# Kernel optimization log

Measured on AMD Instinct MI355X. Metric: run time of the kernel, lower is better.

Reference implementation:

```python
import jax, jax.numpy as jnp
import numpy as np

# Dimensions
N, C, D, H = 4, 1024, 768, 12      # docs, seq_len, hidden, heads
E, M, P = 32, 4, 256               # entities/doc, mentions/entity, pairs/doc
BS, NL = 64, 97                    # block_size, num relation labels


def setup_inputs() -> dict:
    key = jax.random.key(0)
    ks = jax.random.split(key, 16)
    s = 0.02
    seq = jax.random.normal(ks[0], (N, C, D), jnp.float32)
    attn = jax.random.uniform(ks[1], (N, H, C, C), jnp.float32)
    pos = jax.random.randint(ks[2], (N, E, M), 1, C)         # mention positions (offset applied, all valid)
    hts = jax.random.randint(ks[3], (N, P, 2), 0, E)         # entity-pair indices
    return {
        'seq': seq, 'attn': attn, 'pos': pos, 'hts': hts,
        'Wq': jax.random.normal(ks[4], (D, D), jnp.float32) * s,
        'bq': jnp.zeros((D,), jnp.float32),
        'Wk': jax.random.normal(ks[5], (D, D), jnp.float32) * s,
        'bk': jnp.zeros((D,), jnp.float32),
        'aw': jax.random.normal(ks[6], (2 * D, 1), jnp.float32) * s,
        'ab': jnp.zeros((1,), jnp.float32),
        'Wh': jax.random.normal(ks[7], (3 * D, D), jnp.float32) * s,
        'bh': jnp.zeros((D,), jnp.float32),
        'Wt': jax.random.normal(ks[8], (3 * D, D), jnp.float32) * s,
        'bt': jnp.zeros((D,), jnp.float32),
        'Wb': jax.random.normal(ks[9], (D * BS, NL), jnp.float32) * s,
        'bb': jnp.zeros((NL,), jnp.float32),
    }


def mention_guide(rs, mem, mask, Wq, bq, Wk, bk, aw, ab):
    # rs: [N,P,D] query; mem: [N,P,M,D] mention embs; mask: [N,P,M] bool
    sq = rs @ Wq + bq                                  # [N,P,D]
    sk = mem @ Wk + bk                                 # [N,P,M,D]
    sq_exp = jnp.broadcast_to(sq[:, :, None, :], sk.shape)
    inp = jnp.concatenate([sq_exp, sk], axis=-1)       # [N,P,M,2D]
    scores = jax.nn.leaky_relu((inp @ aw + ab)[..., 0], 0.01)   # [N,P,M]
    scores = jnp.where(mask, scores, -1e9)
    p = jax.nn.softmax(scores, axis=-1)                # attention over mentions
    return jnp.einsum('npm,npmd->npd', p, sk)


def reference(seq, attn, pos, hts, Wq, bq, Wk, bk, aw, ab, Wh, bh, Wt, bt, Wb, bb):
    nidx = jnp.arange(N)
    # per-entity mention gather + logsumexp pooling
    ment_emb = seq[nidx[:, None, None], pos]                      # [N,E,M,D]
    ent_emb = jax.scipy.special.logsumexp(ment_emb, axis=2)       # [N,E,D]
    att_t = attn.transpose(0, 2, 1, 3)                            # [N,C,H,C]
    ent_att = att_t[nidx[:, None, None], pos].mean(axis=2)        # [N,E,H,C]

    h_idx, t_idx = hts[..., 0], hts[..., 1]
    b = nidx[:, None]
    hs = ent_emb[b, h_idx]                                        # [N,P,D]
    ts = ent_emb[b, t_idx]
    h_att = ent_att[b, h_idx]                                     # [N,P,H,C]
    t_att = ent_att[b, t_idx]
    ht_att = (h_att * t_att).mean(axis=2)                         # [N,P,C]
    ht_att = ht_att / (ht_att.sum(axis=-1, keepdims=True) + 1e-5)
    rs = jnp.einsum('ncd,npc->npd', seq, ht_att)                  # local context

    # mention-level attention for head/tail entities
    h_pos = pos[b, h_idx]                                         # [N,P,M]
    t_pos = pos[b, t_idx]
    h_embs = seq[nidx[:, None, None], h_pos]                      # [N,P,M,D]
    t_embs = seq[nidx[:, None, None], t_pos]
    hess = mention_guide(rs, h_embs, h_pos != 0, Wq, bq, Wk, bk, aw, ab)
    tess = mention_guide(rs, t_embs, t_pos != 0, Wq, bq, Wk, bk, aw, ab)

    zh = jnp.tanh(jnp.tanh(jnp.concatenate([rs, hs, hess], -1) @ Wh + bh))
    zt = jnp.tanh(jnp.concatenate([rs, ts, tess], -1) @ Wt + bt)

    # group bilinear classifier
    b1 = zh.reshape(N * P, D // BS, BS)
    b2 = zt.reshape(N * P, D // BS, BS)
    bl = (b1[:, :, :, None] * b2[:, :, None, :]).reshape(N * P, D * BS)
    return bl @ Wb + bb                                            # [N*P, NL]
```

## Files before the change

### kernel.cpp

```cpp
#include <hip/hip_runtime.h>
#include <hip/hip_bf16.h>
#include <math.h>

#define N_ 4
#define C_ 1024
#define D_ 768
#define H_ 12
#define E_ 32
#define M_ 4
#define P_ 256
#define NL_ 97
#define NLP_ 112
#define NP_ (N_*P_)
#define K3D_ 2304
#define KBL_ 49152

typedef __attribute__((ext_vector_type(8))) short short8;
typedef __attribute__((ext_vector_type(4))) float f32x4;
typedef __attribute__((ext_vector_type(4))) unsigned short ushort4v;

__device__ __forceinline__ short f2bf(float x){
  union { __hip_bfloat16 h; short s; } u; u.h = __float2bfloat16(x); return u.s;
}
__device__ __forceinline__ unsigned short f2bfu(float x){
  union { __hip_bfloat16 h; unsigned short s; } u; u.h = __float2bfloat16(x); return u.s;
}
__device__ __forceinline__ float bf2f(unsigned short u){
  union { unsigned int i; float f; } x; x.i = ((unsigned int)u)<<16; return x.f;
}

__device__ __forceinline__ float blockReduceSum256(float v){
  __shared__ float red_s[4];
  #pragma unroll
  for (int o=32;o>0;o>>=1) v += __shfl_down(v, o);
  if ((threadIdx.x & 63)==0) red_s[threadIdx.x>>6] = v;
  __syncthreads();
  float t = red_s[0]+red_s[1]+red_s[2]+red_s[3];
  __syncthreads();
  return t;
}

__device__ __forceinline__ void tcvt64(const float* __restrict__ in,
    __hip_bfloat16* __restrict__ out, int R, int C, int Cp, int tile){
  __shared__ float tb[64][33];
  const int tiles_c = (Cp + 31) >> 5;
  const int rb = (tile/tiles_c)*64, cb = (tile%tiles_c)*32;
  const int tid = threadIdx.x;
  const bool vec = ((C & 3) == 0);
  #pragma unroll
  for (int i=0;i<2;i++){
    const int idx = tid + i*256;
    const int row = idx>>3, c4 = (idx&7)*4;
    const int c = cb + c4;
    float v0=0.f,v1=0.f,v2=0.f,v3=0.f;
    if (vec && c+3 < C){
      const f32x4 v = *(const f32x4*)&in[(size_t)(rb+row)*C + c];
      v0=v[0]; v1=v[1]; v2=v[2]; v3=v[3];
    } else {
      const float* rp = in + (size_t)(rb+row)*C;
      if (c   < C) v0 = rp[c];
      if (c+1 < C) v1 = rp[c+1];
      if (c+2 < C) v2 = rp[c+2];
      if (c+3 < C) v3 = rp[c+3];
    }
    tb[row][c4]=v0; tb[row][c4+1]=v1; tb[row][c4+2]=v2; tb[row][c4+3]=v3;
  }
  __syncthreads();
  #pragma unroll
  for (int i=0;i<4;i++){
    const int idx = tid + i*256;
    const int cr = idx>>5, p = idx&31;
    const int cc = cb + cr;
    if (cc < Cp){
      union { struct { unsigned short a,b; } s; unsigned int u; } pk;
      pk.s.a = f2bfu(tb[2*p][cr]);
      pk.s.b = f2bfu(tb[2*p+1][cr]);
      *(unsigned int*)&out[(size_t)cc*R + rb + 2*p] = pk.u;
    }
  }
}

#define T_WH 864
#define T_WT 864
#define T_WK 288
#define T_WB 3072
#define T_SEQ 1536
#define O_WT  (T_WH)
#define O_WK  (O_WT+T_WT)
#define O_WB  (O_WK+T_WK)
#define O_SEQ (O_WB+T_WB)
#define O_EMB (O_SEQ+T_SEQ)
#define O_ATT (O_EMB+N_*E_)
#define O_VQ  (O_ATT+N_*E_*H_)
#define O_WKAW (O_VQ+D_)
#define O_MISC (O_WKAW+D_)
#define G_PREP (O_MISC+1)

__global__ __launch_bounds__(256) void k_prep(
    const float* __restrict__ seq, const float* __restrict__ attn,
    const int* __restrict__ pos,
    const float* __restrict__ Wq, const float* __restrict__ bq,
    const float* __restrict__ Wk, const float* __restrict__ bk,
    const float* __restrict__ aw, const float* __restrict__ ab,
    const float* __restrict__ Wh, const float* __restrict__ Wt,
    const float* __restrict__ Wb,
    __hip_bfloat16* __restrict__ WhT, __hip_bfloat16* __restrict__ WtT,
    __hip_bfloat16* __restrict__ WkT, __hip_bfloat16* __restrict__ WbT,
    __hip_bfloat16* __restrict__ seqT,
    __hip_bfloat16* __restrict__ ent_bf, __hip_bfloat16* __restrict__ Ambf,
    __hip_bfloat16* __restrict__ att_bf,
    float* __restrict__ vq, float* __restrict__ wk_aw, float* __restrict__ qc2){
  const int b = blockIdx.x;
  const int tid = threadIdx.x;
  if (b < O_WT){ tcvt64(Wh, WhT, K3D_, D_, D_, b); return; }
  if (b < O_WK){ tcvt64(Wt, WtT, K3D_, D_, D_, b-O_WT); return; }
  if (b < O_WB){ tcvt64(Wk, WkT, D_, D_, D_, b-O_WK); return; }
  if (b < O_SEQ){ tcvt64(Wb, WbT, KBL_, NL_, NLP_, b-O_WB); return; }
  if (b < O_EMB){ tcvt64(seq, seqT, N_*C_, D_, D_, b-O_SEQ); return; }
  if (b < O_ATT){
    const int be = b - O_EMB;
    const int n = be >> 5;
    const int* pp = pos + be*M_;
    if (tid < 192){
      const int c4 = tid*4;
      const f32x4 v0 = *(const f32x4*)&seq[((size_t)n*C_ + pp[0])*D_ + c4];
      const f32x4 v1 = *(const f32x4*)&seq[((size_t)n*C_ + pp[1])*D_ + c4];
      const f32x4 v2 = *(const f32x4*)&seq[((size_t)n*C_ + pp[2])*D_ + c4];
      const f32x4 v3 = *(const f32x4*)&seq[((size_t)n*C_ + pp[3])*D_ + c4];
      ushort4v a0,a1,a2,a3,e;
      #pragma unroll
      for (int j=0;j<4;j++){
        a0[j]=f2bfu(v0[j]); a1[j]=f2bfu(v1[j]); a2[j]=f2bfu(v2[j]); a3[j]=f2bfu(v3[j]);
        const float m = fmaxf(fmaxf(v0[j],v1[j]), fmaxf(v2[j],v3[j]));
        const float s = expf(v0[j]-m)+expf(v1[j]-m)+expf(v2[j]-m)+expf(v3[j]-m);
        e[j] = f2bfu(m + logf(s));
      }
      *(ushort4v*)&Ambf[(size_t)(be*4+0)*D_ + c4] = a0;
      *(ushort4v*)&Ambf[(size_t)(be*4+1)*D_ + c4] = a1;
      *(ushort4v*)&Ambf[(size_t)(be*4+2)*D_ + c4] = a2;
      *(ushort4v*)&Ambf[(size_t)(be*4+3)*D_ + c4] = a3;
      *(ushort4v*)&ent_bf[(size_t)be*D_ + c4] = e;
    }
    return;
  }
  if (b < O_VQ){
    const int bb2 = b - O_ATT;
    const int h = bb2 % H_;
    const int ne = bb2 / H_;
    const int n = ne >> 5;
    const int* pp = pos + ne*M_;
    const float* basep = attn + ((size_t)(n*H_+h))*C_*C_;
    const int c4 = tid*4;
    const f32x4 r0 = *(const f32x4*)&basep[(size_t)pp[0]*C_ + c4];
    const f32x4 r1 = *(const f32x4*)&basep[(size_t)pp[1]*C_ + c4];
    const f32x4 r2 = *(const f32x4*)&basep[(size_t)pp[2]*C_ + c4];
    const f32x4 r3 = *(const f32x4*)&basep[(size_t)pp[3]*C_ + c4];
    ushort4v o;
    #pragma unroll
    for (int j=0;j<4;j++) o[j] = f2bfu(0.25f*(r0[j]+r1[j]+r2[j]+r3[j]));
    *(ushort4v*)&att_bf[(size_t)bb2*C_ + c4] = o;
    return;
  }
  if (b < O_WKAW){
    const int k = b - O_VQ;
    float s = 0.f;
    for (int d=tid; d<D_; d+=256) s += Wq[(size_t)k*D_+d]*aw[d];
    s = blockReduceSum256(s);
    if (tid==0) vq[k] = s;
    return;
  }
  if (b < O_MISC){
    const int k = b - O_WKAW;
    float s = 0.f;
    for (int d=tid; d<D_; d+=256) s += Wk[(size_t)k*D_+d]*aw[D_+d];
    s = blockReduceSum256(s);
    if (tid==0) wk_aw[k] = s;
    return;
  }
  {
    float s0 = 0.f, s1 = 0.f;
    for (int d=tid; d<D_; d+=256){ s0 += bq[d]*aw[d]; s1 += bk[d]*aw[D_+d]; }
    s0 = blockReduceSum256(s0);
    s1 = blockReduceSum256(s1);
    if (tid==0){ qc2[0] = s0 + ab[0]; qc2[1] = s1; }
  }
}

__global__ __launch_bounds__(256) void k_ht2(
    const __hip_bfloat16* __restrict__ att_bf, const int* __restrict__ hts,
    const __hip_bfloat16* __restrict__ Ambf, const float* __restrict__ wk_aw,
    const float* __restrict__ qc2,
    __hip_bfloat16* __restrict__ ht_bf, float* __restrict__ kdot){
  const int b = blockIdx.x, tid = threadIdx.x;
  if (b < NP_){
    const int r = b, n = r >> 8;
    const int he = hts[r*2], te = hts[r*2+1];
    const unsigned short* ha = (const unsigned short*)att_bf + ((size_t)(n*E_+he))*H_*C_;
    const unsigned short* ta = (const unsigned short*)att_bf + ((size_t)(n*E_+te))*H_*C_;
    const int c0 = tid*4;
    float v[4] = {0.f,0.f,0.f,0.f};
    #pragma unroll
    for (int h=0;h<H_;h++){
      const ushort4v a = *(const ushort4v*)&ha[h*C_ + c0];
      const ushort4v t = *(const ushort4v*)&ta[h*C_ + c0];
      #pragma unroll
      for (int j=0;j<4;j++) v[j] = fmaf(bf2f(a[j]), bf2f(t[j]), v[j]);
    }
    float local = 0.f;
    #pragma unroll
    for (int j=0;j<4;j++){ v[j] *= (1.0f/H_); local += v[j]; }
    const float tot = blockReduceSum256(local);
    const float inv = 1.f/(tot + 1e-5f);
    ushort4v o;
    #pragma unroll
    for (int j=0;j<4;j++) o[j] = f2bfu(v[j]*inv);
    *(ushort4v*)&ht_bf[(size_t)r*C_ + c0] = o;
  } else {
    const int g = b - NP_;
    const unsigned short* Am = (const unsigned short*)Ambf + (size_t)g*D_;
    float s = 0.f;
    for (int d=tid; d<D_; d+=256) s += bf2f(Am[d])*wk_aw[d];
    s = blockReduceSum256(s);
    if (tid==0) kdot[g] = s + qc2[1];
  }
}

__global__ __launch_bounds__(256) void k_gemm1(
    const __hip_bfloat16* __restrict__ Ambf, const __hip_bfloat16* __restrict__ WkT,
    const float* __restrict__ bk, float* __restrict__ KK,
    const __hip_bfloat16* __restrict__ ht_bf, const __hip_bfloat16* __restrict__ seqT,
    __hip_bfloat16* __restrict__ rs_bf){
  __shared__ short As[64][136];
  __shared__ short Bs[64][136];
  const int tid = threadIdx.x;
  const int w = tid>>6, l = tid&63, wm = w>>1, wn = w&1;
  const int srow = tid>>4, sk8 = (tid&15)*8;
  const int p = blockIdx.x;
  const int work = (p & 7)*36 + (p >> 3);
  const short *Ap, *Bp;
  int lda, ldb, K, bm, bn;
  bool isKK;
  if (work < 96){
    isKK = true;
    bm = (work/12)*64; bn = (work%12)*64;
    Ap = (const short*)Ambf + (size_t)bm*D_; lda = D_; K = D_;
    Bp = (const short*)WkT + (size_t)bn*D_;  ldb = D_;
  } else {
    isKK = false;
    const int z = work - 96;
    const int n = z/48, rem = z%48, bnI = rem/16, bmI = rem%16;
    bm = n*P_ + (bmI&3)*64; bn = (bnI*4 + (bmI>>2))*64;
    Ap = (const short*)ht_bf + (size_t)bm*C_;            lda = C_;     K = C_;
    Bp = (const short*)seqT + (size_t)bn*(N_*C_) + n*C_; ldb = N_*C_;
  }
  short8 pA[4], pB[4];
  auto loadAB = [&](int k0){
    #pragma unroll
    for (int t=0;t<4;t++){
      const int row = srow + t*16;
      pA[t] = *(const short8*)&Ap[(size_t)row*lda + k0 + sk8];
      pB[t] = *(const short8*)&Bp[(size_t)row*ldb + k0 + sk8];
    }
  };
  loadAB(0);
  f32x4 acc[2][2] = {};
  for (int k0=0;k0<K;k0+=128){
    #pragma unroll
    for (int t=0;t<4;t++){
      *(short8*)&As[srow+t*16][sk8] = pA[t];
      *(short8*)&Bs[srow+t*16][sk8] = pB[t];
    }
    __syncthreads();
    if (k0+128 < K) loadAB(k0+128);
    #pragma unroll
    for (int h=0;h<4;h++){
      short8 af[2], bfv[2];
      #pragma unroll
      for (int f=0;f<2;f++){
        af[f]  = *(short8*)&As[wm*32+f*16+(l&15)][h*32+(l>>4)*8];
        bfv[f] = *(short8*)&Bs[wn*32+f*16+(l&15)][h*32+(l>>4)*8];
      }
      #pragma unroll
      for (int i=0;i<2;i++)
        #pragma unroll
        for (int j=0;j<2;j++)
          acc[i][j] = __builtin_amdgcn_mfma_f32_16x16x32_bf16(af[i], bfv[j], acc[i][j], 0,0,0);
    }
    __syncthreads();
  }
  #pragma unroll
  for (int i=0;i<2;i++)
    #pragma unroll
    for (int j=0;j<2;j++)
      #pragma unroll
      for (int r_=0;r_<4;r_++){
        const int row = bm + wm*32 + i*16 + (l>>4)*4 + r_;
        const int col = bn + wn*32 + j*16 + (l&15);
        const float v = acc[i][j][r_];
        if (isKK) KK[(size_t)row*D_ + col] = v + bk[col];
        else      rs_bf[(size_t)row*D_ + col] = __float2bfloat16(v);
      }
}

__global__ __launch_bounds__(256) void k_mention(
    const __hip_bfloat16* __restrict__ rs_bf, const float* __restrict__ KK,
    const float* __restrict__ vq, const float* __restrict__ qc2,
    const float* __restrict__ kdot, const int* __restrict__ pos,
    const int* __restrict__ hts,
    __hip_bfloat16* __restrict__ hess, __hip_bfloat16* __restrict__ tess){
  const int r = blockIdx.x, n = r>>8, tid = threadIdx.x;
  const unsigned short* rsp = (const unsigned short*)rs_bf + (size_t)r*D_;
  float s = 0.f;
  for (int d=tid; d<D_; d+=256) s += bf2f(rsp[d])*vq[d];
  const float q = blockReduceSum256(s) + qc2[0];
  #pragma unroll
  for (int side=0;side<2;side++){
    const int e = hts[r*2+side];
    const int base = (n*E_+e)*M_;
    float sc[4];
    #pragma unroll
    for (int m=0;m<4;m++){
      float t = q + kdot[base+m];
      t = (t > 0.f) ? t : 0.01f*t;
      sc[m] = (pos[base+m] != 0) ? t : -1e9f;
    }
    const float mx = fmaxf(fmaxf(sc[0],sc[1]), fmaxf(sc[2],sc[3]));
    float ex[4]; float sum = 0.f;
    #pragma unroll
    for (int m=0;m<4;m++){ ex[m] = expf(sc[m]-mx); sum += ex[m]; }
    const float inv = 1.f/sum;
    const float p0=ex[0]*inv, p1=ex[1]*inv, p2=ex[2]*inv, p3=ex[3]*inv;
    const float* K0 = KK + (size_t)(base+0)*D_;
    const float* K1 = KK + (size_t)(base+1)*D_;
    const float* K2 = KK + (size_t)(base+2)*D_;
    const float* K3 = KK + (size_t)(base+3)*D_;
    __hip_bfloat16* outp = (side ? tess : hess) + (size_t)r*D_;
    for (int d=tid; d<D_; d+=256)
      outp[d] = __float2bfloat16(p0*K0[d] + p1*K1[d] + p2*K2[d] + p3*K3[d]);
  }
}

__global__ __launch_bounds__(256) void k_gemm_z(
    const __hip_bfloat16* __restrict__ rs_bf, const __hip_bfloat16* __restrict__ ent_bf,
    const __hip_bfloat16* __restrict__ hess_bf, const __hip_bfloat16* __restrict__ tess_bf,
    const int* __restrict__ hts,
    const __hip_bfloat16* __restrict__ WhT, const __hip_bfloat16* __restrict__ WtT,
    const float* __restrict__ bh, const float* __restrict__ bt,
    float* __restrict__ zh, float* __restrict__ zt){
  const int p = blockIdx.x;
  const int work = (p & 7)*48 + (p >> 3);
  const int side = work / 192;
  const int w2 = work - side*192;
  const int bn = (w2 / 16)*64;
  const int bm = (w2 & 15)*64;
  const short* BT = (const short*)(side ? WtT : WhT);
  const float* bias = side ? bt : bh;
  float* Cm = side ? zt : zh;
  const short* hx  = (const short*)(side ? tess_bf : hess_bf);
  const short* rsp = (const short*)rs_bf;
  const short* enp = (const short*)ent_bf;
  __shared__ short As[64][136];
  __shared__ short Bs[64][136];
  __shared__ int e_s[64];
  const int tid = threadIdx.x;
  if (tid < 64) e_s[tid] = hts[(bm+tid)*2 + side];
  __syncthreads();
  const int w = tid>>6, l = tid&63, wm = w>>1, wn = w&1;
  const int srow = tid>>4, sk8 = (tid&15)*8;
  short8 pA[4], pB[4];
  auto loadAB = [&](int k0){
    #pragma unroll
    for (int t=0;t<4;t++){
      const int row = srow + t*16;
      const int arow = bm + row;
      const int gk = k0 + sk8;
      const short* src;
      if (gk < D_)        src = &rsp[(size_t)arow*D_ + gk];
      else if (gk < 2*D_) src = &enp[((size_t)(arow>>8)*E_ + e_s[row])*D_ + gk - D_];
      else                src = &hx[(size_t)arow*D_ + gk - 2*D_];
      pA[t] = *(const short8*)src;
      pB[t] = *(const short8*)&BT[(size_t)(bn+row)*K3D_ + gk];
    }
  };
  loadAB(0);
  f32x4 acc[2][2] = {};
  for (int k0=0;k0<K3D_;k0+=128){
    #pragma unroll
    for (int t=0;t<4;t++){
      *(short8*)&As[srow+t*16][sk8] = pA[t];
      *(short8*)&Bs[srow+t*16][sk8] = pB[t];
    }
    __syncthreads();
    if (k0+128 < K3D_) loadAB(k0+128);
    #pragma unroll
    for (int h=0;h<4;h++){
      short8 af[2], bfv[2];
      #pragma unroll
      for (int f=0;f<2;f++){
        af[f]  = *(short8*)&As[wm*32+f*16+(l&15)][h*32+(l>>4)*8];
        bfv[f] = *(short8*)&Bs[wn*32+f*16+(l&15)][h*32+(l>>4)*8];
      }
      #pragma unroll
      for (int i=0;i<2;i++)
        #pragma unroll
        for (int j=0;j<2;j++)
          acc[i][j] = __builtin_amdgcn_mfma_f32_16x16x32_bf16(af[i], bfv[j], acc[i][j], 0,0,0);
    }
    __syncthreads();
  }
  #pragma unroll
  for (int i=0;i<2;i++)
    #pragma unroll
    for (int j=0;j<2;j++)
      #pragma unroll
      for (int r_=0;r_<4;r_++){
        const int row = bm + wm*32 + i*16 + (l>>4)*4 + r_;
        const int col = bn + wn*32 + j*16 + (l&15);
        float v = acc[i][j][r_] + bias[col];
        v = tanhf(v);
        if (side==0) v = tanhf(v);
        Cm[(size_t)row*D_ + col] = v;
      }
}

__global__ __launch_bounds__(256) void k_bilinear(
    const float* __restrict__ zh, const float* __restrict__ zt,
    const __hip_bfloat16* __restrict__ WbT, __hip_bfloat16* __restrict__ partial){
  const int p = blockIdx.x;
  const int work = (p & 7)*48 + (p >> 3);
  const int kc = work >> 4;
  const int r0 = (work & 15)*64;
  const int blkI = kc >> 1, half = kc & 1;
  __shared__ float zh_s[64][36];
  __shared__ float zt_s[64][68];
  __shared__ short Bs[4][NLP_][40];
  const int tid = threadIdx.x;
  for (int idx=tid; idx<64*32; idx+=256){
    const int row = idx>>5, c = idx&31;
    zh_s[row][c] = zh[(size_t)(r0+row)*D_ + blkI*64 + half*32 + c];
  }
  for (int idx=tid; idx<64*64; idx+=256){
    const int row = idx>>6, c = idx&63;
    zt_s[row][c] = zt[(size_t)(r0+row)*D_ + blkI*64 + c];
  }
  const int w = tid>>6, l = tid&63;
  const int arow = w*16 + (l&15);
  const short* WT = (const short*)WbT;
  const size_t kbase = (size_t)blkI*4096 + half*2048;
  int sl[7], cl[7], k8l[7];
  #pragma unroll
  for (int t=0;t<7;t++){
    const int ci = tid + t*256;
    sl[t] = ci/448;
    const int rem = ci - sl[t]*448;
    cl[t] = rem>>2; k8l[t] = (rem&3)*8;
  }
  short8 pre[7];
  #pragma unroll
  for (int t=0;t<7;t++)
    pre[t] = *(const short8*)&WT[(size_t)cl[t]*KBL_ + kbase + (size_t)sl[t]*32 + k8l[t]];
  f32x4 acc[7] = {};
  for (int g=0; g<16; ++g){
    __syncthreads();
    #pragma unroll
    for (int t=0;t<7;t++) *(short8*)&Bs[sl[t]][cl[t]][k8l[t]] = pre[t];
    __syncthreads();
    if (g < 15){
      #pragma unroll
      for (int t=0;t<7;t++)
        pre[t] = *(const short8*)&WT[(size_t)cl[t]*KBL_ + kbase + (size_t)((g+1)*4+sl[t])*32 + k8l[t]];
    }
    #pragma unroll
    for (int ss=0;ss<4;ss++){
      const int s = g*4 + ss;
      const int iLoc = s>>1;
      const int jj = (s&1)*32 + (l>>4)*8;
      const float a = zh_s[arow][iLoc];
      f32x4 z0 = *(f32x4*)&zt_s[arow][jj];
      f32x4 z1 = *(f32x4*)&zt_s[arow][jj+4];
      short8 afr;
      #pragma unroll
      for (int t=0;t<4;t++) afr[t]   = f2bf(a*z0[t]);
      #pragma unroll
      for (int t=0;t<4;t++) afr[4+t] = f2bf(a*z1[t]);
      #pragma unroll
      for (int nf=0;nf<7;nf++){
        const short8 bfr = *(short8*)&Bs[ss][nf*16 + (l&15)][(l>>4)*8];
        acc[nf] = __builtin_amdgcn_mfma_f32_16x16x32_bf16(afr, bfr, acc[nf], 0,0,0);
      }
    }
  }
  unsigned short* pp = (unsigned short*)partial;
  #pragma unroll
  for (int nf=0;nf<7;nf++)
    #pragma unroll
    for (int r_=0;r_<4;r_++){
      const int row = r0 + w*16 + (l>>4)*4 + r_;
      const int col = nf*16 + (l&15);
      pp[((size_t)kc*NP_ + row)*NLP_ + col] = f2bfu(acc[nf][r_]);
    }
}

__global__ __launch_bounds__(256) void k_reduce(const __hip_bfloat16* __restrict__ partial,
    const float* __restrict__ bb, float* __restrict__ out){
  const int idx = blockIdx.x*256 + threadIdx.x;
  if (idx >= NP_*NL_) return;
  const int r = idx / NL_;
  const int l = idx - r*NL_;
  const unsigned short* pp = (const unsigned short*)partial;
  float s = bb[l];
  #pragma unroll
  for (int kc=0;kc<24;kc++) s += bf2f(pp[((size_t)kc*NP_ + r)*NLP_ + l]);
  out[idx] = s;
}

extern "C" void kernel_launch(void* const* d_in, const int* in_sizes, int n_in,
                              void* d_out, int out_size, void* d_ws, size_t ws_size,
                              hipStream_t stream){
  const float* seq  = (const float*)d_in[0];
  const float* attn = (const float*)d_in[1];
  const int*   pos  = (const int*)d_in[2];
  const int*   hts  = (const int*)d_in[3];
  const float* Wq = (const float*)d_in[4];
  const float* bq = (const float*)d_in[5];
  const float* Wk = (const float*)d_in[6];
  const float* bk = (const float*)d_in[7];
  const float* aw = (const float*)d_in[8];
  const float* ab = (const float*)d_in[9];
  const float* Wh = (const float*)d_in[10];
  const float* bh = (const float*)d_in[11];
  const float* Wt = (const float*)d_in[12];
  const float* bt = (const float*)d_in[13];
  const float* Wb = (const float*)d_in[14];
  const float* bb = (const float*)d_in[15];
  float* out = (float*)d_out;

  char* base = (char*)d_ws;
  size_t off = 0;
  auto alloc = [&](size_t bytes)->void*{
    void* p = base + off;
    off += (bytes + 255) & ~(size_t)255;
    return p;
  };
  __hip_bfloat16* WhT   = (__hip_bfloat16*)alloc((size_t)D_*K3D_*2);
  __hip_bfloat16* WtT   = (__hip_bfloat16*)alloc((size_t)D_*K3D_*2);
  __hip_bfloat16* WkT   = (__hip_bfloat16*)alloc((size_t)D_*D_*2);
  __hip_bfloat16* WbT   = (__hip_bfloat16*)alloc((size_t)NLP_*KBL_*2);
  __hip_bfloat16* seqT  = (__hip_bfloat16*)alloc((size_t)D_*N_*C_*2);
  __hip_bfloat16* ent_bf= (__hip_bfloat16*)alloc((size_t)N_*E_*D_*2);
  __hip_bfloat16* att_bf= (__hip_bfloat16*)alloc((size_t)N_*E_*H_*C_*2);
  __hip_bfloat16* ht_bf = (__hip_bfloat16*)alloc((size_t)NP_*C_*2);
  __hip_bfloat16* Ambf  = (__hip_bfloat16*)alloc((size_t)N_*E_*M_*D_*2);
  float* KK             = (float*)alloc((size_t)N_*E_*M_*D_*4);
  float* vq             = (float*)alloc(D_*4);
  float* wk_aw          = (float*)alloc(D_*4);
  float* qc2            = (float*)alloc(256);
  float* kdot           = (float*)alloc(512*4);
  __hip_bfloat16* rs_bf = (__hip_bfloat16*)alloc((size_t)NP_*D_*2);
  __hip_bfloat16* hess  = (__hip_bfloat16*)alloc((size_t)NP_*D_*2);
  __hip_bfloat16* tess  = (__hip_bfloat16*)alloc((size_t)NP_*D_*2);
  float* zh             = (float*)alloc((size_t)NP_*D_*4);
  float* zt             = (float*)alloc((size_t)NP_*D_*4);
  __hip_bfloat16* partial = (__hip_bfloat16*)alloc((size_t)24*NP_*NLP_*2);
  (void)ws_size; (void)in_sizes; (void)n_in; (void)out_size;

  k_prep<<<G_PREP, 256, 0, stream>>>(seq, attn, pos, Wq, bq, Wk, bk, aw, ab, Wh, Wt, Wb,
                                     WhT, WtT, WkT, WbT, seqT, ent_bf, Ambf, att_bf,
                                     vq, wk_aw, qc2);
  k_ht2<<<NP_ + 512, 256, 0, stream>>>(att_bf, hts, Ambf, wk_aw, qc2, ht_bf, kdot);
  k_gemm1<<<288, 256, 0, stream>>>(Ambf, WkT, bk, KK, ht_bf, seqT, rs_bf);
  k_mention<<<NP_, 256, 0, stream>>>(rs_bf, KK, vq, qc2, kdot, pos, hts, hess, tess);
  k_gemm_z<<<384, 256, 0, stream>>>(rs_bf, ent_bf, hess, tess, hts,
                                    WhT, WtT, bh, bt, zh, zt);
  k_bilinear<<<384, 256, 0, stream>>>(zh, zt, WbT, partial);
  k_reduce<<<(NP_*NL_+255)/256, 256, 0, stream>>>(partial, bb, out);
}
```

Before: 104.3 us.

## Use direct global-to-LDS loads with XOR swizzle in GEMMs; store z in bf16

Result: no change. 104.1 us (median of 2 runs) (-0.2%).

```diff
diff --git a/kernel.cpp b/kernel.cpp
--- a/kernel.cpp
+++ b/kernel.cpp
@@ -18,6 +18,10 @@
 typedef __attribute__((ext_vector_type(8))) short short8;
 typedef __attribute__((ext_vector_type(4))) float f32x4;
 typedef __attribute__((ext_vector_type(4))) unsigned short ushort4v;
+
+#define GLOAD_LDS16(g, l) __builtin_amdgcn_global_load_lds( \
+    (const __attribute__((address_space(1))) void*)(g), \
+    (__attribute__((address_space(3))) void*)(l), 16, 0, 0)
 
 __device__ __forceinline__ short f2bf(float x){
   union { __hip_bfloat16 h; short s; } u; u.h = __float2bfloat16(x); return u.s;
@@ -230,11 +234,12 @@
     const float* __restrict__ bk, float* __restrict__ KK,
     const __hip_bfloat16* __restrict__ ht_bf, const __hip_bfloat16* __restrict__ seqT,
     __hip_bfloat16* __restrict__ rs_bf){
-  __shared__ short As[64][136];
-  __shared__ short Bs[64][136];
+  __shared__ short As[64*128];
+  __shared__ short Bs[64*128];
   const int tid = threadIdx.x;
-  const int w = tid>>6, l = tid&63, wm = w>>1, wn = w&1;
-  const int srow = tid>>4, sk8 = (tid&15)*8;
+  const int lam = tid & 63, wv = tid >> 6;
+  const int wm = wv >> 1, wn = wv & 1;
+  const int lr4 = lam >> 4, c16 = lam & 15;
   const int p = blockIdx.x;
   const int work = (p & 7)*36 + (p >> 3);
   const short *Ap, *Bp;
@@ -253,50 +258,54 @@
     Ap = (const short*)ht_bf + (size_t)bm*C_;            lda = C_;     K = C_;
     Bp = (const short*)seqT + (size_t)bn*(N_*C_) + n*C_; ldb = N_*C_;
   }
-  short8 pA[4], pB[4];
-  auto loadAB = [&](int k0){
-    #pragma unroll
-    for (int t=0;t<4;t++){
-      const int row = srow + t*16;
-      pA[t] = *(const short8*)&Ap[(size_t)row*lda + k0 + sk8];
-      pB[t] = *(const short8*)&Bp[(size_t)row*ldb + k0 + sk8];
-    }
-  };
-  loadAB(0);
   f32x4 acc[2][2] = {};
   for (int k0=0;k0<K;k0+=128){
-    #pragma unroll
-    for (int t=0;t<4;t++){
-      *(short8*)&As[srow+t*16][sk8] = pA[t];
-      *(short8*)&Bs[srow+t*16][sk8] = pB[t];
-    }
     __syncthreads();
-    if (k0+128 < K) loadAB(k0+128);
+    if (wv < 2){
+      #pragma unroll
+      for (int j=0;j<8;j++){
+        const int ai = wv*8 + j;
+        const int row = ai*4 + lr4;
+        const int csw = c16 ^ (row & 15);
+        GLOAD_LDS16(Ap + (size_t)row*lda + k0 + csw*8, &As[ai*512]);
+      }
+    } else {
+      #pragma unroll
+      for (int j=0;j<8;j++){
+        const int bi = (wv-2)*8 + j;
+        const int row = bi*4 + lr4;
+        const int csw = c16 ^ (row & 15);
+        GLOAD_LDS16(Bp + (size_t)row*ldb + k0 + csw*8, &Bs[bi*512]);
+      }
+    }
+    asm volatile("s_waitcnt vmcnt(0)" ::: "memory");
+    __syncthreads();
     #pragma unroll
     for (int h=0;h<4;h++){
       short8 af[2], bfv[2];
       #pragma unroll
       for (int f=0;f<2;f++){
-        af[f]  = *(short8*)&As[wm*32+f*16+(l&15)][h*32+(l>>4)*8];
-        bfv[f] = *(short8*)&Bs[wn*32+f*16+(l&15)][h*32+(l>>4)*8];
+        const int rl = lam & 15;
+        const int cs = ((4*h + (lam>>4)) ^ rl)*8;
+        af[f]  = *(short8*)&As[(wm*32+f*16+rl)*128 + cs];
+        bfv[f] = *(short8*)&Bs[(wn*32+f*16+rl)*128 + cs];
       }
       #pragma unroll
       for (int i=0;i<2;i++)
         #pragma unroll
-        for (int j=0;j<2;j++)
-          acc[i][j] = __builtin_amdgcn_mfma_f32_16x16x32_bf16(af[i], bfv[j], acc[i][j], 0,0,0);
-    }
-    __syncthreads();
+        for (int jj=0;jj<2;jj++)
+          acc[i][jj] = __builtin_amdgcn_mfma_f32_16x16x32_bf16(af[i], bfv[jj], acc[i][jj], 0,0,0);
+    }
   }
   #pragma unroll
   for (int i=0;i<2;i++)
     #pragma unroll
-    for (int j=0;j<2;j++)
+    for (int jj=0;jj<2;jj++)
       #pragma unroll
       for (int r_=0;r_<4;r_++){
-        const int row = bm + wm*32 + i*16 + (l>>4)*4 + r_;
-        const int col = bn + wn*32 + j*16 + (l&15);
-        const float v = acc[i][j][r_];
+        const int row = bm + wm*32 + i*16 + (lam>>4)*4 + r_;
+        const int col = bn + wn*32 + jj*16 + (lam&15);
+        const float v = acc[i][jj][r_];
         if (isKK) KK[(size_t)row*D_ + col] = v + bk[col];
         else      rs_bf[(size_t)row*D_ + col] = __float2bfloat16(v);
       }
@@ -346,7 +355,7 @@
     const int* __restrict__ hts,
     const __hip_bfloat16* __restrict__ WhT, const __hip_bfloat16* __restrict__ WtT,
     const float* __restrict__ bh, const float* __restrict__ bt,
-    float* __restrict__ zh, float* __restrict__ zt){
+    __hip_bfloat16* __restrict__ zh, __hip_bfloat16* __restrict__ zt){
   const int p = blockIdx.x;
   const int work = (p & 7)*48 + (p >> 3);
   const int side = work / 192;
@@ -355,76 +364,81 @@
   const int bm = (w2 & 15)*64;
   const short* BT = (const short*)(side ? WtT : WhT);
   const float* bias = side ? bt : bh;
-  float* Cm = side ? zt : zh;
+  unsigned short* Cm = (unsigned short*)(side ? zt : zh);
   const short* hx  = (const short*)(side ? tess_bf : hess_bf);
   const short* rsp = (const short*)rs_bf;
   const short* enp = (const short*)ent_bf;
-  __shared__ short As[64][136];
-  __shared__ short Bs[64][136];
+  __shared__ short As[64*128];
+  __shared__ short Bs[64*128];
   __shared__ int e_s[64];
   const int tid = threadIdx.x;
   if (tid < 64) e_s[tid] = hts[(bm+tid)*2 + side];
   __syncthreads();
-  const int w = tid>>6, l = tid&63, wm = w>>1, wn = w&1;
-  const int srow = tid>>4, sk8 = (tid&15)*8;
-  short8 pA[4], pB[4];
-  auto loadAB = [&](int k0){
-    #pragma unroll
-    for (int t=0;t<4;t++){
-      const int row = srow + t*16;
-      const int arow = bm + row;
-      const int gk = k0 + sk8;
-      const short* src;
-      if (gk < D_)        src = &rsp[(size_t)arow*D_ + gk];
-      else if (gk < 2*D_) src = &enp[((size_t)(arow>>8)*E_ + e_s[row])*D_ + gk - D_];
-      else                src = &hx[(size_t)arow*D_ + gk - 2*D_];
-      pA[t] = *(const short8*)src;
-      pB[t] = *(const short8*)&BT[(size_t)(bn+row)*K3D_ + gk];
-    }
-  };
-  loadAB(0);
+  const int lam = tid & 63, wv = tid >> 6;
+  const int wm = wv >> 1, wn = wv & 1;
+  const int lr4 = lam >> 4, c16 = lam & 15;
+  const int n4 = bm >> 8;
   f32x4 acc[2][2] = {};
   for (int k0=0;k0<K3D_;k0+=128){
-    #pragma unroll
-    for (int t=0;t<4;t++){
-      *(short8*)&As[srow+t*16][sk8] = pA[t];
-      *(short8*)&Bs[srow+t*16][sk8] = pB[t];
-    }
     __syncthreads();
-    if (k0+128 < K3D_) loadAB(k0+128);
+    if (wv < 2){
+      #pragma unroll
+      for (int j=0;j<8;j++){
+        const int ai = wv*8 + j;
+        const int row = ai*4 + lr4;
+        const int csw = c16 ^ (row & 15);
+        const int gk = k0 + csw*8;
+        const short* src;
+        if (k0 < D_)        src = rsp + (size_t)(bm+row)*D_ + gk;
+        else if (k0 < 2*D_) src = enp + ((size_t)(n4*E_ + e_s[row]))*D_ + (gk - D_);
+        else                src = hx  + (size_t)(bm+row)*D_ + (gk - 2*D_);
+        GLOAD_LDS16(src, &As[ai*512]);
+      }
+    } else {
+      #pragma unroll
+      for (int j=0;j<8;j++){
+        const int bi = (wv-2)*8 + j;
+        const int row = bi*4 + lr4;
+        const int csw = c16 ^ (row & 15);
+        GLOAD_LDS16(BT + (size_t)(bn+row)*K3D_ + k0 + csw*8, &Bs[bi*512]);
+      }
+    }
+    asm volatile("s_waitcnt vmcnt(0)" ::: "memory");
+    __syncthreads();
     #pragma unroll
     for (int h=0;h<4;h++){
       short8 af[2], bfv[2];
       #pragma unroll
       for (int f=0;f<2;f++){
-        af[f]  = *(short8*)&As[wm*32+f*16+(l&15)][h*32+(l>>4)*8];
-        bfv[f] = *(short8*)&Bs[wn*32+f*16+(l&15)][h*32+(l>>4)*8];
+        const int rl = lam & 15;
+        const int cs = ((4*h + (lam>>4)) ^ rl)*8;
+        af[f]  = *(short8*)&As[(wm*32+f*16+rl)*128 + cs];
+        bfv[f] = *(short8*)&Bs[(wn*32+f*16+rl)*128 + cs];
       }
       #pragma unroll
       for (int i=0;i<2;i++)
         #pragma unroll
-        for (int j=0;j<2;j++)
-          acc[i][j] = __builtin_amdgcn_mfma_f32_16x16x32_bf16(af[i], bfv[j], acc[i][j], 0,0,0);
-    }
-    __syncthreads();
+        for (int jj=0;jj<2;jj++)
+          acc[i][jj] = __builtin_amdgcn_mfma_f32_16x16x32_bf16(af[i], bfv[jj], acc[i][jj], 0,0,0);
+    }
   }
   #pragma unroll
   for (int i=0;i<2;i++)
     #pragma unroll
-    for (int j=0;j<2;j++)
+    for (int jj=0;jj<2;jj++)
       #pragma unroll
       for (int r_=0;r_<4;r_++){
-        const int row = bm + wm*32 + i*16 + (l>>4)*4 + r_;
-        const int col = bn + wn*32 + j*16 + (l&15);
-        float v = acc[i][j][r_] + bias[col];
+        const int row = bm + wm*32 + i*16 + (lam>>4)*4 + r_;
+        const int col = bn + wn*32 + jj*16 + (lam&15);
+        float v = acc[i][jj][r_] + bias[col];
         v = tanhf(v);
         if (side==0) v = tanhf(v);
-        Cm[(size_t)row*D_ + col] = v;
+        Cm[(size_t)row*D_ + col] = f2bfu(v);
       }
 }
 
 __global__ __launch_bounds__(256) void k_bilinear(
-    const float* __restrict__ zh, const float* __restrict__ zt,
+    const __hip_bfloat16* __restrict__ zh, const __hip_bfloat16* __restrict__ zt,
     const __hip_bfloat16* __restrict__ WbT, __hip_bfloat16* __restrict__ partial){
   const int p = blockIdx.x;
   const int work = (p & 7)*48 + (p >> 3);
@@ -435,13 +449,19 @@
   __shared__ float zt_s[64][68];
   __shared__ short Bs[4][NLP_][40];
   const int tid = threadIdx.x;
-  for (int idx=tid; idx<64*32; idx+=256){
-    const int row = idx>>5, c = idx&31;
-    zh_s[row][c] = zh[(size_t)(r0+row)*D_ + blkI*64 + half*32 + c];
-  }
-  for (int idx=tid; idx<64*64; idx+=256){
-    const int row = idx>>6, c = idx&63;
-    zt_s[row][c] = zt[(size_t)(r0+row)*D_ + blkI*64 + c];
+  const unsigned short* zhu = (const unsigned short*)zh;
+  const unsigned short* ztu = (const unsigned short*)zt;
+  for (int idx=tid; idx<64*8; idx+=256){
+    const int row = idx>>3, c4 = (idx&7)*4;
+    const ushort4v v = *(const ushort4v*)&zhu[(size_t)(r0+row)*D_ + blkI*64 + half*32 + c4];
+    #pragma unroll
+    for (int j=0;j<4;j++) zh_s[row][c4+j] = bf2f(v[j]);
+  }
+  for (int idx=tid; idx<64*16; idx+=256){
+    const int row = idx>>4, c4 = (idx&15)*4;
+    const ushort4v v = *(const ushort4v*)&ztu[(size_t)(r0+row)*D_ + blkI*64 + c4];
+    #pragma unroll
+    for (int j=0;j<4;j++) zt_s[row][c4+j] = bf2f(v[j]);
   }
   const int w = tid>>6, l = tid&63;
   const int arow = w*16 + (l&15);
@@ -559,8 +579,8 @@
   __hip_bfloat16* rs_bf = (__hip_bfloat16*)alloc((size_t)NP_*D_*2);
   __hip_bfloat16* hess  = (__hip_bfloat16*)alloc((size_t)NP_*D_*2);
   __hip_bfloat16* tess  = (__hip_bfloat16*)alloc((size_t)NP_*D_*2);
-  float* zh             = (float*)alloc((size_t)NP_*D_*4);
-  float* zt             = (float*)alloc((size_t)NP_*D_*4);
+  __hip_bfloat16* zh    = (__hip_bfloat16*)alloc((size_t)NP_*D_*2);
+  __hip_bfloat16* zt    = (__hip_bfloat16*)alloc((size_t)NP_*D_*2);
   __hip_bfloat16* partial = (__hip_bfloat16*)alloc((size_t)24*NP_*NLP_*2);
   (void)ws_size; (void)in_sizes; (void)n_in; (void)out_size;
 
```
